# Kernel tuning notes

Hardware: AMD Instinct MI355X
Metric: run time of the kernel (lower is better)

Reference implementation:

```python
import jax, jax.numpy as jnp
import numpy as np

SLOPE = 0.2  # leaky_relu_slope for both LVC block and kernel predictor (passed through)
DILATIONS = (1, 3, 9, 27)
HOP = 256
STRIDE = 8
IN_CH = 32
KSZ = 3  # conv_kernel_size


def conv1d(x, w, b, dilation=1, padding=0):
    # x: (B,C,T), w: (O,I,K) torch layout
    y = jax.lax.conv_general_dilated(
        x, w, window_strides=(1,), padding=[(padding, padding)],
        rhs_dilation=(dilation,), dimension_numbers=('NCH', 'OIH', 'NCH'))
    return y + b[None, :, None]


def conv_transpose1d(x, w, b, stride, padding, output_padding=0):
    # w: torch ConvTranspose1d layout (Cin, Cout, K)
    w_ = jnp.flip(w, -1).transpose(1, 0, 2)  # (Cout, Cin, K)
    K = w.shape[2]
    pad = (K - 1 - padding, K - 1 - padding + output_padding)
    y = jax.lax.conv_general_dilated(
        x, w_, window_strides=(1,), padding=[pad],
        lhs_dilation=(stride,), dimension_numbers=('NCH', 'OIH', 'NCH'))
    return y + b[None, :, None]


def lrelu(x, slope=SLOPE):
    return jnp.where(x >= 0, x, slope * x)


def location_variable_convolution(x, kernel, bias, hop):
    # x: (B,C,T), kernel: (B,C,O,k,L), bias: (B,O,L); T == L*hop; dilation==1 path
    B, C, T = x.shape
    _, _, O, k, L = kernel.shape
    pad = (k - 1) // 2
    xp = jnp.pad(x, ((0, 0), (0, 0), (pad, pad)))
    # gather per-segment sliding windows: (L, hop, k) index into time axis
    idx = (jnp.arange(L)[:, None, None] * hop
           + jnp.arange(hop)[None, :, None]
           + jnp.arange(k)[None, None, :])
    xw = xp[:, :, idx]  # (B, C, L, hop, k)
    o = jnp.einsum('bclsk,bcokl->bols', xw, kernel)  # (B, O, L, hop)
    o = o + bias[:, :, :, None]
    return o.reshape(B, O, L * hop)


def kernel_predictor(spec, kp_in_w, kp_in_b, rb_w1, rb_b1, rb_w2, rb_b2,
                     kern_w, kern_b, bias_w, bias_b):
    B, _, L = spec.shape
    h = conv1d(spec, kp_in_w, kp_in_b, padding=2)  # k=5, pad=2
    for i in range(3):  # num_blocks = 3
        r = h
        h = conv1d(h, rb_w1[i], rb_b1[i], padding=1)
        h = lrelu(h)
        h = conv1d(h, rb_w2[i], rb_b2[i], padding=1)
        h = lrelu(h) + r
    kh = conv1d(h, kern_w, kern_b, padding=1)
    bh = conv1d(h, bias_w, bias_b, padding=1)
    n_layers = len(DILATIONS)
    kernels = kh.reshape(B, n_layers, IN_CH, 2 * IN_CH, KSZ, L)
    biases = bh.reshape(B, n_layers, 2 * IN_CH, L)
    return kernels, biases


def reference(hidden_states, spectrogram, convt_w, convt_b, kp_in_w, kp_in_b,
              rb_w1, rb_b1, rb_w2, rb_b2, kern_w, kern_b, bias_w, bias_b,
              lvc_w, lvc_b):
    h = conv_transpose1d(hidden_states, convt_w, convt_b,
                         stride=STRIDE, padding=STRIDE // 2 + STRIDE % 2,
                         output_padding=STRIDE % 2)
    kernels, biases = kernel_predictor(spectrogram, kp_in_w, kp_in_b,
                                       rb_w1, rb_b1, rb_w2, rb_b2,
                                       kern_w, kern_b, bias_w, bias_b)
    for i, d in enumerate(DILATIONS):
        r = h
        h = lrelu(h)
        h = conv1d(h, lvc_w[i], lvc_b[i], dilation=d, padding=d * (KSZ - 1) // 2)
        h = lrelu(h)
        h = location_variable_convolution(h, kernels[:, i], biases[:, i], HOP)
        h = jax.nn.sigmoid(h[:, :IN_CH, :]) * jnp.tanh(h[:, IN_CH:, :]) + r
    return h


def setup_inputs() -> dict:
    key = jax.random.key(0)
    ks = jax.random.split(key, 12)
    B, COND, L, H = 4, 100, 256, 64
    T = L * HOP  # 65536 output samples
    s = jnp.float32(0.02)
    d = {}
    d['hidden_states'] = jax.random.normal(ks[0], (B, IN_CH, T // STRIDE), jnp.float32)
    d['spectrogram'] = jax.random.normal(ks[1], (B, COND, L), jnp.float32)
    d['convt_w'] = jax.random.normal(ks[2], (IN_CH, IN_CH, 2 * STRIDE), jnp.float32) * s
    d['convt_b'] = jnp.zeros((IN_CH,), jnp.float32)
    d['kp_in_w'] = jax.random.normal(ks[3], (H, COND, 5), jnp.float32) * s
    d['kp_in_b'] = jnp.zeros((H,), jnp.float32)
    d['rb_w1'] = jax.random.normal(ks[4], (3, H, H, 3), jnp.float32) * s
    d['rb_b1'] = jnp.zeros((3, H), jnp.float32)
    d['rb_w2'] = jax.random.normal(ks[5], (3, H, H, 3), jnp.float32) * s
    d['rb_b2'] = jnp.zeros((3, H), jnp.float32)
    KC = IN_CH * 2 * IN_CH * KSZ * len(DILATIONS)  # 24576
    d['kern_w'] = jax.random.normal(ks[6], (KC, H, 3), jnp.float32) * s
    d['kern_b'] = jnp.zeros((KC,), jnp.float32)
    BC = 2 * IN_CH * len(DILATIONS)  # 256
    d['bias_w'] = jax.random.normal(ks[7], (BC, H, 3), jnp.float32) * s
    d['bias_b'] = jnp.zeros((BC,), jnp.float32)
    d['lvc_w'] = jax.random.normal(ks[8], (len(DILATIONS), IN_CH, IN_CH, 3), jnp.float32) * s
    d['lvc_b'] = jnp.zeros((len(DILATIONS), IN_CH), jnp.float32)
    return d
```

## Files before the change

kernel.cpp:

```cpp
#include <hip/hip_runtime.h>
#include <math.h>

#define NB 4
#define T 65536
#define TIN 8192
#define LL 256
#define KCL 6144

__device__ __forceinline__ float lrelu_f(float v) { return v >= 0.f ? v : 0.2f * v; }

union Phase1LDS {
    struct { float xs[32][264]; float wm[64][128]; } cvt;
    struct { float hs[64][56]; float xsp[20][56]; float wt[192][68]; } trk;
};

__global__ void __launch_bounds__(512) phase1(
    const float* __restrict__ x, const float* __restrict__ cw,
    const float* __restrict__ cbias, float* __restrict__ hout,
    const float* __restrict__ spec,
    const float* __restrict__ kp_in_w, const float* __restrict__ kp_in_b,
    const float* __restrict__ rb_w1, const float* __restrict__ rb_b1,
    const float* __restrict__ rb_w2, const float* __restrict__ rb_b2,
    float* __restrict__ kp_h) {
    __shared__ Phase1LDS u;
    const int bid = blockIdx.x;
    const int tid = threadIdx.x;
    const int lane = tid & 63, wv = tid >> 6;

    if (bid < 264) {
        const int bx = bid % 33;
        const int rr = bid / 33;
        const int mtp = rr & 1;
        const int b = rr >> 1;
        const int s0base = bx * 256;
        float (*xs)[264] = u.cvt.xs;
        float (*wm)[128] = u.cvt.wm;

        const float* xb = x + (size_t)b * 32 * TIN;
        for (int idx = tid; idx < 32 * 64; idx += 512) {
            int c = idx >> 6, q = idx & 63;
            int p = s0base + q * 4;
            float4 v = (p + 3 < TIN) ? *(const float4*)(xb + c * TIN + p)
                                     : make_float4(0.f, 0.f, 0.f, 0.f);
            *(float4*)&xs[c][4 + 4 * q] = v;
        }
        if (tid < 32) {
            int p = s0base - 1;
            xs[tid][3] = (p >= 0) ? xb[tid * TIN + p] : 0.f;
        }
        for (int idx = tid; idx < 8192; idx += 512) {
            int i = idx >> 7, mm = idx & 127;
            int oo = mtp * 16 + (mm >> 3), k0 = mm & 7;
            wm[i][mm] = (i < 32) ? cw[i * 512 + oo * 16 + k0]
                                 : cw[(i - 32) * 512 + oo * 16 + k0 + 8];
        }
        __syncthreads();

        float acc[2][8][4];
#pragma unroll
        for (int ol = 0; ol < 2; ++ol) {
            float bo = cbias[mtp * 16 + wv * 2 + ol];
#pragma unroll
            for (int k0 = 0; k0 < 8; ++k0)
#pragma unroll
                for (int si = 0; si < 4; ++si) acc[ol][k0][si] = bo;
        }

        for (int c = 0; c < 32; ++c) {
            float xm1[4], x0[4];
#pragma unroll
            for (int si = 0; si < 4; ++si) {
                xm1[si] = xs[c][lane + si * 64 + 3];
                x0[si]  = xs[c][lane + si * 64 + 4];
            }
            float w0[16], w1[16];
#pragma unroll
            for (int q = 0; q < 4; ++q) {
                *(float4*)&w0[q * 4] = *(const float4*)&wm[c][wv * 16 + q * 4];
                *(float4*)&w1[q * 4] = *(const float4*)&wm[32 + c][wv * 16 + q * 4];
            }
#pragma unroll
            for (int ol = 0; ol < 2; ++ol)
#pragma unroll
                for (int k0 = 0; k0 < 8; ++k0)
#pragma unroll
                    for (int si = 0; si < 4; ++si)
                        acc[ol][k0][si] += x0[si] * w0[ol * 8 + k0] + xm1[si] * w1[ol * 8 + k0];
        }

#pragma unroll
        for (int ol = 0; ol < 2; ++ol) {
            float* ob = hout + ((size_t)b * 32 + mtp * 16 + wv * 2 + ol) * T;
#pragma unroll
            for (int si = 0; si < 4; ++si) {
                int tb = (s0base + lane + si * 64) * 8 - 4;
                if (tb >= 0 && tb < T)
                    *(float4*)(ob + tb) = make_float4(acc[ol][0][si], acc[ol][1][si],
                                                      acc[ol][2][si], acc[ol][3][si]);
                if (tb + 4 >= 0 && tb + 4 < T)
                    *(float4*)(ob + tb + 4) = make_float4(acc[ol][4][si], acc[ol][5][si],
                                                          acc[ol][6][si], acc[ol][7][si]);
            }
        }
        return;
    }

    const int tb = bid - 264;
    const int lq = tb & 7, b = tb >> 3;
    const int j = lane;
    const int oc0 = wv * 8;
    const int l0 = lq * 32;
    const int labs = l0 - 9 + j;
    const bool lvalid = (labs >= 0 && labs < 256);

    float (*hs)[56] = u.trk.hs;
    float (*xsp)[56] = u.trk.xsp;
    float (*wt)[68] = u.trk.wt;

    float pw[24];
    float px[3];

    auto pf_kpin = [&](int cc) {
#pragma unroll
        for (int t = 0; t < 13; ++t) {
            int idx = t * 512 + tid;
            pw[t] = 0.f;
            if (idx < 6400) pw[t] = kp_in_w[(size_t)(idx / 100) * 500 + cc * 100 + (idx % 100)];
        }
    };
    auto wr_kpin = [&]() {
#pragma unroll
        for (int t = 0; t < 13; ++t) {
            int idx = t * 512 + tid;
            if (idx < 6400) wt[idx % 100][idx / 100] = pw[t];
        }
    };
    auto pf_xsp = [&](int cc) {
#pragma unroll
        for (int t = 0; t < 3; ++t) {
            int idx = t * 512 + tid;
            px[t] = 0.f;
            if (idx < 1120) {
                int c = idx / 56, jj = idx - c * 56;
                int l = l0 - 9 + jj;
                if (l >= 0 && l < 256)
                    px[t] = spec[((size_t)b * 100 + cc * 20 + c) * LL + l];
            }
        }
    };
    auto wr_xsp = [&]() {
#pragma unroll
        for (int t = 0; t < 3; ++t) {
            int idx = t * 512 + tid;
            if (idx < 1120) xsp[idx / 56][idx % 56] = px[t];
        }
    };
    auto pf_w192 = [&](const float* src) {
#pragma unroll
        for (int t = 0; t < 24; ++t) pw[t] = src[t * 512 + tid];
    };
    auto wr_w192 = [&]() {
#pragma unroll
        for (int t = 0; t < 24; ++t) {
            int idx = t * 512 + tid;
            wt[idx % 192][idx / 192] = pw[t];
        }
    };
    auto conv64 = [&](int jlo, int jhi, const float* bptr, float* a) {
#pragma unroll
        for (int oi = 0; oi < 8; ++oi) a[oi] = bptr[oc0 + oi];
        if (j >= jlo && j < jhi) {
            for (int c = 0; c < 64; ++c) {
                float x0 = hs[c][j - 1], x1 = hs[c][j], x2 = hs[c][j + 1];
#pragma unroll
                for (int k = 0; k < 3; ++k) {
                    float xk = (k == 0) ? x0 : (k == 1) ? x1 : x2;
                    float w8[8];
                    *(float4*)&w8[0] = *(const float4*)&wt[c * 3 + k][oc0];
                    *(float4*)&w8[4] = *(const float4*)&wt[c * 3 + k][oc0 + 4];
#pragma unroll
                    for (int oi = 0; oi < 8; ++oi) a[oi] += xk * w8[oi];
                }
            }
        }
    };

    pf_kpin(0); pf_xsp(0);
    wr_kpin(); wr_xsp();
    __syncthreads();

    float acc[8];
#pragma unroll
    for (int oi = 0; oi < 8; ++oi) acc[oi] = kp_in_b[oc0 + oi];

    for (int cc = 0; cc < 5; ++cc) {
        if (cc < 4) { pf_kpin(cc + 1); pf_xsp(cc + 1); }
        else        { pf_w192(rb_w1); }
        if (j >= 2 && j < 48) {
            for (int c = 0; c < 20; ++c) {
                float x5[5];
#pragma unroll
                for (int u2 = 0; u2 < 5; ++u2) x5[u2] = xsp[c][j - 2 + u2];
#pragma unroll
                for (int k = 0; k < 5; ++k) {
                    float w8[8];
                    *(float4*)&w8[0] = *(const float4*)&wt[c * 5 + k][oc0];
                    *(float4*)&w8[4] = *(const float4*)&wt[c * 5 + k][oc0 + 4];
#pragma unroll
                    for (int oi = 0; oi < 8; ++oi) acc[oi] += x5[k] * w8[oi];
                }
            }
        }
        if (cc == 4 && j >= 2 && j < 48) {
#pragma unroll
            for (int oi = 0; oi < 8; ++oi) hs[oc0 + oi][j] = lvalid ? acc[oi] : 0.f;
        }
        __syncthreads();
        if (cc < 4) { wr_kpin(); wr_xsp(); }
        else        { wr_w192(); }
        __syncthreads();
    }

    for (int i = 0; i < 3; ++i) {
        const int jlo1 = 3 + 2 * i, jhi1 = 47 - 2 * i;
        const int jlo2 = jlo1 + 1, jhi2 = jhi1 - 1;
        float r[8];
        if (j >= jlo2 && j < jhi2) {
#pragma unroll
            for (int oi = 0; oi < 8; ++oi) r[oi] = hs[oc0 + oi][j];
        }
        pf_w192(rb_w2 + (size_t)i * 12288);
        float a1[8];
        conv64(jlo1, jhi1, rb_b1 + i * 64, a1);
        __syncthreads();
        if (j >= jlo1 && j < jhi1) {
#pragma unroll
            for (int oi = 0; oi < 8; ++oi) hs[oc0 + oi][j] = lvalid ? lrelu_f(a1[oi]) : 0.f;
        }
        wr_w192();
        __syncthreads();
        if (i < 2) pf_w192(rb_w1 + (size_t)(i + 1) * 12288);
        float a2[8];
        conv64(jlo2, jhi2, rb_b2 + i * 64, a2);
        __syncthreads();
        if (j >= jlo2 && j < jhi2) {
#pragma unroll
            for (int oi = 0; oi < 8; ++oi) hs[oc0 + oi][j] = lvalid ? (lrelu_f(a2[oi]) + r[oi]) : 0.f;
        }
        if (i < 2) wr_w192();
        __syncthreads();
    }

    for (int idx = tid; idx < 64 * 32; idx += 512) {
        int c = idx >> 5, jj = idx & 31;
        kp_h[((size_t)b * 64 + c) * LL + l0 + jj] = hs[c][9 + jj];
    }
}

__global__ void __launch_bounds__(256, 3) kern_head(const float* __restrict__ kp_h,
                                                    const float* __restrict__ kw,
                                                    const float* __restrict__ kb,
                                                    const float* __restrict__ bias_w,
                                                    const float* __restrict__ bias_b,
                                                    float* __restrict__ kh,
                                                    float* __restrict__ bh, int layer) {
    const int bx = blockIdx.x, b = blockIdx.y;
    const bool isbias = (bx >= 192);
    const int tid = threadIdx.x, lane = tid & 63, wv = tid >> 6;
    __shared__ float xs[32][264];
    __shared__ float ws[96][36];

    int g = 0, oc0 = 0, ci = 0, kk = 0, ocb0 = 0;
    const float* wsrc;
    size_t wrow0;
    int wstride;
    if (!isbias) {
        g = bx >> 1; oc0 = (bx & 1) * 32;
        ci = g / 3; kk = g - ci * 3;
        wsrc = kw + (size_t)layer * KCL * 192;
        wrow0 = (size_t)((ci * 64 + oc0) * 3 + kk) * 192;
        wstride = 576;
    } else {
        ocb0 = (bx - 192) * 32;
        wsrc = bias_w;
        wrow0 = (size_t)ocb0 * 192;
        wstride = 192;
    }

    float acc[8][4];
#pragma unroll
    for (int oi = 0; oi < 8; ++oi) {
        float bv = isbias ? bias_b[ocb0 + wv * 8 + oi]
                          : kb[layer * KCL + (ci * 64 + oc0 + wv * 8 + oi) * 3 + kk];
#pragma unroll
        for (int si = 0; si < 4; ++si) acc[oi][si] = bv;
    }

    for (int half = 0; half < 2; ++half) {
        const int hc0 = half * 32;
        __syncthreads();
        for (int idx = tid; idx < 32 * 64; idx += 256) {
            int c = idx >> 6, q = idx & 63;
            *(float4*)&xs[c][4 + 4 * q] =
                *(const float4*)(kp_h + ((size_t)b * 64 + hc0 + c) * LL + 4 * q);
        }
        if (tid < 32) { xs[tid][3] = 0.f; xs[tid][260] = 0.f; }
        for (int idx = tid; idx < 3072; idx += 256) {
            int ocl = idx / 96, jj = idx - ocl * 96;
            ws[jj][ocl] = wsrc[wrow0 + (size_t)ocl * wstride + hc0 * 3 + jj];
        }
        __syncthreads();
        for (int c = 0; c < 32; ++c) {
#pragma unroll
            for (int t = 0; t < 3; ++t) {
                float wv8[8];
                *(float4*)&wv8[0] = *(const float4*)&ws[c * 3 + t][wv * 8];
                *(float4*)&wv8[4] = *(const float4*)&ws[c * 3 + t][wv * 8 + 4];
                float xv[4];
#pragma unroll
                for (int si = 0; si < 4; ++si) xv[si] = xs[c][lane + si * 64 + t + 3];
#pragma unroll
                for (int oi = 0; oi < 8; ++oi)
#pragma unroll
                    for (int si = 0; si < 4; ++si)
                        acc[oi][si] += wv8[oi] * xv[si];
            }
        }
    }

    if (!isbias) {
#pragma unroll
        for (int si = 0; si < 4; ++si) {
            int l = lane + si * 64;
            float* op = kh + ((size_t)b * LL + l) * KCL + g * 64 + oc0 + wv * 8;
            *(float4*)(op)     = make_float4(acc[0][si], acc[1][si], acc[2][si], acc[3][si]);
            *(float4*)(op + 4) = make_float4(acc[4][si], acc[5][si], acc[6][si], acc[7][si]);
        }
    } else {
#pragma unroll
        for (int oi = 0; oi < 8; ++oi) {
            float* op = bh + ((size_t)b * 256 + ocb0 + wv * 8 + oi) * LL;
#pragma unroll
            for (int si = 0; si < 4; ++si)
                op[lane + si * 64] = acc[oi][si];
        }
    }
}

__global__ void __launch_bounds__(512, 4) layer_fused(
    const float* __restrict__ kh, const float* __restrict__ bh,
    const float* __restrict__ w, const float* __restrict__ bias,
    const float* __restrict__ hin, float* __restrict__ hout,
    int layer, int dil) {
    const int l = blockIdx.x, b = blockIdx.y;
    const int tid = threadIdx.x, lane = tid & 63, wv = tid >> 6;
    const int t0 = l * 256;
    __shared__ float xh[32][316];
    __shared__ float ks[KCL];
    __shared__ float ws[96][36];

    const float* hb = hin + (size_t)b * 32 * T;
    for (int idx = tid; idx < 32 * 64; idx += 512) {
        int c = idx >> 6, q = idx & 63;
        float4 v = *(const float4*)(hb + (size_t)c * T + t0 + 4 * q);
        *(float4*)&xh[c][32 + 4 * q] = make_float4(lrelu_f(v.x), lrelu_f(v.y),
                                                   lrelu_f(v.z), lrelu_f(v.w));
    }
    for (int idx = tid; idx < 32 * 60; idx += 512) {
        int c = idx / 60, r = idx - c * 60;
        int jj = (r < 32) ? r : (256 + r);
        int t = t0 + jj - 32;
        xh[c][jj] = (t >= 0 && t < T) ? lrelu_f(hb[(size_t)c * T + t]) : 0.f;
    }
    {
        const float4* kp = (const float4*)(kh + ((size_t)b * LL + l) * KCL);
        float4* kd = (float4*)ks;
        for (int idx = tid; idx < KCL / 4; idx += 512) kd[idx] = kp[idx];
    }
    for (int idx = tid; idx < 3072; idx += 512) {
        int oc = idx / 96, ck = idx - oc * 96;
        ws[ck][oc] = w[oc * 96 + ck];
    }
    __syncthreads();

    const int oc4 = wv * 4;
    float yv[5][4];
    {
        float a[5][4];
#pragma unroll
        for (int oi = 0; oi < 4; ++oi) {
            float bv = bias[oc4 + oi];
#pragma unroll
            for (int si = 0; si < 5; ++si) a[si][oi] = bv;
        }
        for (int c = 0; c < 32; ++c) {
#pragma unroll
            for (int k = 0; k < 3; ++k) {
                float4 wq = *(const float4*)&ws[c * 3 + k][oc4];
                float xv[5];
#pragma unroll
                for (int si = 0; si < 5; ++si) {
                    int col = lane + si * 64;
                    int colc = (col < 258) ? col : 257;
                    xv[si] = xh[c][colc + 31 + (k - 1) * dil];
                }
#pragma unroll
                for (int si = 0; si < 5; ++si) {
                    a[si][0] += xv[si] * wq.x;
                    a[si][1] += xv[si] * wq.y;
                    a[si][2] += xv[si] * wq.z;
                    a[si][3] += xv[si] * wq.w;
                }
            }
        }
#pragma unroll
        for (int si = 0; si < 5; ++si) {
            int t = t0 - 1 + lane + si * 64;
            bool tval = (t >= 0 && t < T);
#pragma unroll
            for (int oi = 0; oi < 4; ++oi)
                yv[si][oi] = tval ? lrelu_f(a[si][oi]) : 0.f;
        }
    }
    __syncthreads();

#pragma unroll
    for (int si = 0; si < 5; ++si) {
        int col = lane + si * 64;
        if (col < 258) {
#pragma unroll
            for (int oi = 0; oi < 4; ++oi) xh[oc4 + oi][col + 31] = yv[si][oi];
        }
    }
    __syncthreads();

    const int oc8 = (wv & 3) * 8;
    const int sh  = wv >> 2;
    float acc_a[8][2], acc_g[8][2];
#pragma unroll
    for (int oi = 0; oi < 8; ++oi) {
        float ba = bh[((size_t)b * 256 + layer * 64 + oc8 + oi) * LL + l];
        float bg = bh[((size_t)b * 256 + layer * 64 + 32 + oc8 + oi) * LL + l];
#pragma unroll
        for (int si = 0; si < 2; ++si) { acc_a[oi][si] = ba; acc_g[oi][si] = bg; }
    }

    for (int c = 0; c < 32; ++c) {
#pragma unroll
        for (int k = 0; k < 3; ++k) {
            const float* kr = ks + (c * 3 + k) * 64;
            float wa[8], wg[8];
            *(float4*)&wa[0] = *(const float4*)(kr + oc8);
            *(float4*)&wa[4] = *(const float4*)(kr + oc8 + 4);
            *(float4*)&wg[0] = *(const float4*)(kr + 32 + oc8);
            *(float4*)&wg[4] = *(const float4*)(kr + 32 + oc8 + 4);
            float xv2[2];
#pragma unroll
            for (int si = 0; si < 2; ++si) {
                int s = lane + (sh * 2 + si) * 64;
                xv2[si] = xh[c][s + k + 31];
            }
#pragma unroll
            for (int oi = 0; oi < 8; ++oi)
#pragma unroll
                for (int si = 0; si < 2; ++si) {
                    acc_a[oi][si] += wa[oi] * xv2[si];
                    acc_g[oi][si] += wg[oi] * xv2[si];
                }
        }
    }

#pragma unroll
    for (int oi = 0; oi < 8; ++oi) {
        const float* hip = hin + ((size_t)b * 32 + oc8 + oi) * T + t0;
        float* hop = hout + ((size_t)b * 32 + oc8 + oi) * T + t0;
#pragma unroll
        for (int si = 0; si < 2; ++si) {
            int s = lane + (sh * 2 + si) * 64;
            float a = acc_a[oi][si], g = acc_g[oi][si];
            float sg = 1.f / (1.f + __expf(-a));
            float th = tanhf(g);
            hop[s] = sg * th + hip[s];
        }
    }
}

extern "C" void kernel_launch(void* const* d_in, const int* in_sizes, int n_in,
                              void* d_out, int out_size, void* d_ws, size_t ws_size,
                              hipStream_t stream) {
    const float* hidden  = (const float*)d_in[0];
    const float* spec    = (const float*)d_in[1];
    const float* convt_w = (const float*)d_in[2];
    const float* convt_b = (const float*)d_in[3];
    const float* kp_in_w = (const float*)d_in[4];
    const float* kp_in_b = (const float*)d_in[5];
    const float* rb_w1   = (const float*)d_in[6];
    const float* rb_b1   = (const float*)d_in[7];
    const float* rb_w2   = (const float*)d_in[8];
    const float* rb_b2   = (const float*)d_in[9];
    const float* kern_w  = (const float*)d_in[10];
    const float* kern_b  = (const float*)d_in[11];
    const float* bias_w  = (const float*)d_in[12];
    const float* bias_b  = (const float*)d_in[13];
    const float* lvc_w   = (const float*)d_in[14];
    const float* lvc_b   = (const float*)d_in[15];

    float* wsp = (float*)d_ws;
    float* h_ws     = wsp;
    float* kh_layer = h_ws + (size_t)NB * 32 * T;
    float* bh       = kh_layer + (size_t)NB * LL * KCL;
    float* kp_h     = bh + (size_t)NB * 256 * LL;

    float* h0 = (float*)d_out;
    float* h1 = h_ws;

    phase1<<<dim3(296), 512, 0, stream>>>(hidden, convt_w, convt_b, h0,
                                          spec, kp_in_w, kp_in_b,
                                          rb_w1, rb_b1, rb_w2, rb_b2, kp_h);

    static const int dil[4] = {1, 3, 9, 27};
    float* hin = h0;
    float* hout = h1;
    for (int layer = 0; layer < 4; ++layer) {
        kern_head<<<dim3(layer == 0 ? 200 : 192, NB), 256, 0, stream>>>(
            kp_h, kern_w, kern_b, bias_w, bias_b, kh_layer, bh, layer);
        layer_fused<<<dim3(LL, NB), 512, 0, stream>>>(
            kh_layer, bh, lvc_w + (size_t)layer * 32 * 32 * 3, lvc_b + layer * 32,
            hin, hout, layer, dil[layer]);
        float* tmp = hin; hin = hout; hout = tmp;
    }
}
```

Before: 723.7 us.

## Remap kernel-predictor threads to output channels and split LVC pre-conv by channel halves

The kernel-predictor tail of phase1 now assigns one output channel per lane and eight time positions per wave. Weights are read straight from global memory into registers in place of the LDS-staged transposed weight buffer, and the software prefetch pipeline is removed. The LVC-layer pre-convolution is restructured so that each wave computes 8 output channels over half the input channels, and the two halves are reduced through LDS. The aim is fewer LDS weight reads and better register reuse, at the cost of heavy register pressure (96-float weight arrays) and extra barriers.

```diff
diff --git a/kernel.cpp b/kernel.cpp
--- a/kernel.cpp
+++ b/kernel.cpp
@@ -9,9 +9,9 @@
 
 __device__ __forceinline__ float lrelu_f(float v) { return v >= 0.f ? v : 0.2f * v; }
 
-union Phase1LDS {
+union __align__(16) Phase1LDS {
     struct { float xs[32][264]; float wm[64][128]; } cvt;
-    struct { float hs[64][56]; float xsp[20][56]; float wt[192][68]; } trk;
+    struct { float hs[64][68]; float xsp[20][68]; } trk;
 };
 
 __global__ void __launch_bounds__(512) phase1(
@@ -105,155 +105,161 @@
         return;
     }
 
-    const int tb = bid - 264;
-    const int lq = tb & 7, b = tb >> 3;
-    const int j = lane;
-    const int oc0 = wv * 8;
+    const int tb2 = bid - 264;
+    const int lq = tb2 & 7, b = tb2 >> 3;
+    const int oc = lane;
+    const int j0 = wv * 8;
     const int l0 = lq * 32;
-    const int labs = l0 - 9 + j;
-    const bool lvalid = (labs >= 0 && labs < 256);
-
-    float (*hs)[56] = u.trk.hs;
-    float (*xsp)[56] = u.trk.xsp;
-    float (*wt)[68] = u.trk.wt;
-
-    float pw[24];
-    float px[3];
-
-    auto pf_kpin = [&](int cc) {
-#pragma unroll
-        for (int t = 0; t < 13; ++t) {
-            int idx = t * 512 + tid;
-            pw[t] = 0.f;
-            if (idx < 6400) pw[t] = kp_in_w[(size_t)(idx / 100) * 500 + cc * 100 + (idx % 100)];
-        }
-    };
-    auto wr_kpin = [&]() {
-#pragma unroll
-        for (int t = 0; t < 13; ++t) {
-            int idx = t * 512 + tid;
-            if (idx < 6400) wt[idx % 100][idx / 100] = pw[t];
-        }
-    };
-    auto pf_xsp = [&](int cc) {
-#pragma unroll
-        for (int t = 0; t < 3; ++t) {
-            int idx = t * 512 + tid;
-            px[t] = 0.f;
-            if (idx < 1120) {
-                int c = idx / 56, jj = idx - c * 56;
-                int l = l0 - 9 + jj;
-                if (l >= 0 && l < 256)
-                    px[t] = spec[((size_t)b * 100 + cc * 20 + c) * LL + l];
-            }
-        }
-    };
-    auto wr_xsp = [&]() {
-#pragma unroll
-        for (int t = 0; t < 3; ++t) {
-            int idx = t * 512 + tid;
-            if (idx < 1120) xsp[idx / 56][idx % 56] = px[t];
-        }
-    };
-    auto pf_w192 = [&](const float* src) {
-#pragma unroll
-        for (int t = 0; t < 24; ++t) pw[t] = src[t * 512 + tid];
-    };
-    auto wr_w192 = [&]() {
-#pragma unroll
-        for (int t = 0; t < 24; ++t) {
-            int idx = t * 512 + tid;
-            wt[idx % 192][idx / 192] = pw[t];
-        }
-    };
-    auto conv64 = [&](int jlo, int jhi, const float* bptr, float* a) {
-#pragma unroll
-        for (int oi = 0; oi < 8; ++oi) a[oi] = bptr[oc0 + oi];
-        if (j >= jlo && j < jhi) {
-            for (int c = 0; c < 64; ++c) {
-                float x0 = hs[c][j - 1], x1 = hs[c][j], x2 = hs[c][j + 1];
-#pragma unroll
-                for (int k = 0; k < 3; ++k) {
-                    float xk = (k == 0) ? x0 : (k == 1) ? x1 : x2;
-                    float w8[8];
-                    *(float4*)&w8[0] = *(const float4*)&wt[c * 3 + k][oc0];
-                    *(float4*)&w8[4] = *(const float4*)&wt[c * 3 + k][oc0 + 4];
-#pragma unroll
-                    for (int oi = 0; oi < 8; ++oi) a[oi] += xk * w8[oi];
-                }
-            }
-        }
-    };
-
-    pf_kpin(0); pf_xsp(0);
-    wr_kpin(); wr_xsp();
+    const bool active = (j0 < 48);
+
+    float (*hs)[68] = u.trk.hs;
+    float (*xsp)[68] = u.trk.xsp;
+
+    for (int idx = tid; idx < 64 * 68; idx += 512) ((float*)hs)[idx] = 0.f;
+
+    float acc[8];
+#pragma unroll
+    for (int q = 0; q < 8; ++q) acc[q] = kp_in_b[oc];
+
+    for (int cc = 0; cc < 5; ++cc) {
+        __syncthreads();
+        for (int idx = tid; idx < 20 * 68; idx += 512) {
+            int c = idx / 68, v = idx - c * 68;
+            int jj = v - 4;
+            int l = l0 - 9 + jj;
+            float val = 0.f;
+            if (jj >= 0 && jj < 56 && l >= 0 && l < 256)
+                val = spec[((size_t)b * 100 + cc * 20 + c) * LL + l];
+            xsp[c][v] = val;
+        }
+        __syncthreads();
+        if (active) {
+#pragma unroll
+            for (int half = 0; half < 2; ++half) {
+                const int c0 = half ? 12 : 0;
+                const int nc = half ? 8 : 12;
+                float wreg[60];
+                const float* wp = kp_in_w + (size_t)oc * 500 + cc * 100 + c0 * 5;
+#pragma unroll
+                for (int q4 = 0; q4 < 15; ++q4)
+                    if (q4 * 4 < nc * 5)
+                        *(float4*)&wreg[q4 * 4] = *(const float4*)(wp + q4 * 4);
+#pragma unroll
+                for (int c = 0; c < nc; ++c) {
+                    float xw[16];
+                    *(float4*)&xw[0]  = *(const float4*)&xsp[c0 + c][j0];
+                    *(float4*)&xw[4]  = *(const float4*)&xsp[c0 + c][j0 + 4];
+                    *(float4*)&xw[8]  = *(const float4*)&xsp[c0 + c][j0 + 8];
+                    *(float4*)&xw[12] = *(const float4*)&xsp[c0 + c][j0 + 12];
+#pragma unroll
+                    for (int q = 0; q < 8; ++q)
+#pragma unroll
+                        for (int k = 0; k < 5; ++k)
+                            acc[q] += wreg[c * 5 + k] * xw[q + k + 2];
+                }
+            }
+        }
+        __syncthreads();
+    }
+    if (active) {
+#pragma unroll
+        for (int q = 0; q < 8; ++q) {
+            int j = j0 + q;
+            if (j >= 2 && j < 48) {
+                int labs = l0 - 9 + j;
+                hs[oc][2 + j] = (labs >= 0 && labs < 256) ? acc[q] : 0.f;
+            }
+        }
+    }
     __syncthreads();
-
-    float acc[8];
-#pragma unroll
-    for (int oi = 0; oi < 8; ++oi) acc[oi] = kp_in_b[oc0 + oi];
-
-    for (int cc = 0; cc < 5; ++cc) {
-        if (cc < 4) { pf_kpin(cc + 1); pf_xsp(cc + 1); }
-        else        { pf_w192(rb_w1); }
-        if (j >= 2 && j < 48) {
-            for (int c = 0; c < 20; ++c) {
-                float x5[5];
-#pragma unroll
-                for (int u2 = 0; u2 < 5; ++u2) x5[u2] = xsp[c][j - 2 + u2];
-#pragma unroll
-                for (int k = 0; k < 5; ++k) {
-                    float w8[8];
-                    *(float4*)&w8[0] = *(const float4*)&wt[c * 5 + k][oc0];
-                    *(float4*)&w8[4] = *(const float4*)&wt[c * 5 + k][oc0 + 4];
-#pragma unroll
-                    for (int oi = 0; oi < 8; ++oi) acc[oi] += x5[k] * w8[oi];
-                }
-            }
-        }
-        if (cc == 4 && j >= 2 && j < 48) {
-#pragma unroll
-            for (int oi = 0; oi < 8; ++oi) hs[oc0 + oi][j] = lvalid ? acc[oi] : 0.f;
-        }
-        __syncthreads();
-        if (cc < 4) { wr_kpin(); wr_xsp(); }
-        else        { wr_w192(); }
-        __syncthreads();
-    }
 
     for (int i = 0; i < 3; ++i) {
         const int jlo1 = 3 + 2 * i, jhi1 = 47 - 2 * i;
         const int jlo2 = jlo1 + 1, jhi2 = jhi1 - 1;
-        float r[8];
-        if (j >= jlo2 && j < jhi2) {
-#pragma unroll
-            for (int oi = 0; oi < 8; ++oi) r[oi] = hs[oc0 + oi][j];
-        }
-        pf_w192(rb_w2 + (size_t)i * 12288);
-        float a1[8];
-        conv64(jlo1, jhi1, rb_b1 + i * 64, a1);
-        __syncthreads();
-        if (j >= jlo1 && j < jhi1) {
-#pragma unroll
-            for (int oi = 0; oi < 8; ++oi) hs[oc0 + oi][j] = lvalid ? lrelu_f(a1[oi]) : 0.f;
-        }
-        wr_w192();
-        __syncthreads();
-        if (i < 2) pf_w192(rb_w1 + (size_t)(i + 1) * 12288);
+        float r[8], a1[8];
+        if (active) {
+#pragma unroll
+            for (int q = 0; q < 8; ++q) {
+                a1[q] = rb_b1[i * 64 + oc];
+                r[q]  = hs[oc][2 + j0 + q];
+            }
+#pragma unroll
+            for (int half = 0; half < 2; ++half) {
+                float wreg[96];
+                const float* wp = rb_w1 + (size_t)i * 12288 + (size_t)oc * 192 + half * 96;
+#pragma unroll
+                for (int q4 = 0; q4 < 24; ++q4)
+                    *(float4*)&wreg[q4 * 4] = *(const float4*)(wp + q4 * 4);
+#pragma unroll
+                for (int c = 0; c < 32; ++c) {
+                    const int cg = half * 32 + c;
+                    float xw[12];
+                    *(float4*)&xw[0] = *(const float4*)&hs[cg][j0];
+                    *(float4*)&xw[4] = *(const float4*)&hs[cg][j0 + 4];
+                    *(float4*)&xw[8] = *(const float4*)&hs[cg][j0 + 8];
+#pragma unroll
+                    for (int q = 0; q < 8; ++q)
+#pragma unroll
+                        for (int k = 0; k < 3; ++k)
+                            a1[q] += wreg[c * 3 + k] * xw[q + k + 1];
+                }
+            }
+        }
+        __syncthreads();
+        if (active) {
+#pragma unroll
+            for (int q = 0; q < 8; ++q) {
+                int j = j0 + q;
+                if (j >= jlo1 && j < jhi1) {
+                    int labs = l0 - 9 + j;
+                    hs[oc][2 + j] = (labs >= 0 && labs < 256) ? lrelu_f(a1[q]) : 0.f;
+                }
+            }
+        }
+        __syncthreads();
         float a2[8];
-        conv64(jlo2, jhi2, rb_b2 + i * 64, a2);
-        __syncthreads();
-        if (j >= jlo2 && j < jhi2) {
-#pragma unroll
-            for (int oi = 0; oi < 8; ++oi) hs[oc0 + oi][j] = lvalid ? (lrelu_f(a2[oi]) + r[oi]) : 0.f;
-        }
-        if (i < 2) wr_w192();
-        __syncthreads();
-    }
-
-    for (int idx = tid; idx < 64 * 32; idx += 512) {
+        if (active) {
+#pragma unroll
+            for (int q = 0; q < 8; ++q) a2[q] = rb_b2[i * 64 + oc];
+#pragma unroll
+            for (int half = 0; half < 2; ++half) {
+                float wreg[96];
+                const float* wp = rb_w2 + (size_t)i * 12288 + (size_t)oc * 192 + half * 96;
+#pragma unroll
+                for (int q4 = 0; q4 < 24; ++q4)
+                    *(float4*)&wreg[q4 * 4] = *(const float4*)(wp + q4 * 4);
+#pragma unroll
+                for (int c = 0; c < 32; ++c) {
+                    const int cg = half * 32 + c;
+                    float xw[12];
+                    *(float4*)&xw[0] = *(const float4*)&hs[cg][j0];
+                    *(float4*)&xw[4] = *(const float4*)&hs[cg][j0 + 4];
+                    *(float4*)&xw[8] = *(const float4*)&hs[cg][j0 + 8];
+#pragma unroll
+                    for (int q = 0; q < 8; ++q)
+#pragma unroll
+                        for (int k = 0; k < 3; ++k)
+                            a2[q] += wreg[c * 3 + k] * xw[q + k + 1];
+                }
+            }
+        }
+        __syncthreads();
+        if (active) {
+#pragma unroll
+            for (int q = 0; q < 8; ++q) {
+                int j = j0 + q;
+                if (j >= jlo2 && j < jhi2) {
+                    int labs = l0 - 9 + j;
+                    hs[oc][2 + j] = (labs >= 0 && labs < 256) ? (lrelu_f(a2[q]) + r[q]) : 0.f;
+                }
+            }
+        }
+        __syncthreads();
+    }
+
+    for (int idx = tid; idx < 2048; idx += 512) {
         int c = idx >> 5, jj = idx & 31;
-        kp_h[((size_t)b * 64 + c) * LL + l0 + jj] = hs[c][9 + jj];
+        kp_h[((size_t)b * 64 + c) * LL + l0 + jj] = hs[c][11 + jj];
     }
 }
 
@@ -383,53 +389,61 @@
     }
     __syncthreads();
 
-    const int oc4 = wv * 4;
-    float yv[5][4];
-    {
-        float a[5][4];
-#pragma unroll
-        for (int oi = 0; oi < 4; ++oi) {
-            float bv = bias[oc4 + oi];
-#pragma unroll
-            for (int si = 0; si < 5; ++si) a[si][oi] = bv;
-        }
-        for (int c = 0; c < 32; ++c) {
-#pragma unroll
-            for (int k = 0; k < 3; ++k) {
-                float4 wq = *(const float4*)&ws[c * 3 + k][oc4];
-                float xv[5];
-#pragma unroll
-                for (int si = 0; si < 5; ++si) {
-                    int col = lane + si * 64;
-                    int colc = (col < 258) ? col : 257;
-                    xv[si] = xh[c][colc + 31 + (k - 1) * dil];
-                }
-#pragma unroll
-                for (int si = 0; si < 5; ++si) {
-                    a[si][0] += xv[si] * wq.x;
-                    a[si][1] += xv[si] * wq.y;
-                    a[si][2] += xv[si] * wq.z;
-                    a[si][3] += xv[si] * wq.w;
-                }
-            }
-        }
+    const int oc8b = (wv & 3) * 8;
+    const int chb  = wv >> 2;
+    float p[8][5];
+#pragma unroll
+    for (int oi = 0; oi < 8; ++oi)
+#pragma unroll
+        for (int si = 0; si < 5; ++si) p[oi][si] = 0.f;
+
+    for (int c = chb * 16; c < chb * 16 + 16; ++c) {
+#pragma unroll
+        for (int k = 0; k < 3; ++k) {
+            float w8[8];
+            *(float4*)&w8[0] = *(const float4*)&ws[c * 3 + k][oc8b];
+            *(float4*)&w8[4] = *(const float4*)&ws[c * 3 + k][oc8b + 4];
+            float xv[5];
+#pragma unroll
+            for (int si = 0; si < 5; ++si) {
+                int col = lane + si * 64;
+                int colc = (col < 258) ? col : 257;
+                xv[si] = xh[c][colc + 31 + (k - 1) * dil];
+            }
+#pragma unroll
+            for (int oi = 0; oi < 8; ++oi)
+#pragma unroll
+                for (int si = 0; si < 5; ++si)
+                    p[oi][si] += w8[oi] * xv[si];
+        }
+    }
+    __syncthreads();
+
+    if (chb == 0) {
 #pragma unroll
         for (int si = 0; si < 5; ++si) {
-            int t = t0 - 1 + lane + si * 64;
-            bool tval = (t >= 0 && t < T);
-#pragma unroll
-            for (int oi = 0; oi < 4; ++oi)
-                yv[si][oi] = tval ? lrelu_f(a[si][oi]) : 0.f;
+            int col = lane + si * 64;
+            if (col < 258) {
+#pragma unroll
+                for (int oi = 0; oi < 8; ++oi)
+                    xh[oc8b + oi][col + 31] = p[oi][si] + bias[oc8b + oi];
+            }
         }
     }
     __syncthreads();
-
-#pragma unroll
-    for (int si = 0; si < 5; ++si) {
-        int col = lane + si * 64;
-        if (col < 258) {
-#pragma unroll
-            for (int oi = 0; oi < 4; ++oi) xh[oc4 + oi][col + 31] = yv[si][oi];
+    if (chb == 1) {
+#pragma unroll
+        for (int si = 0; si < 5; ++si) {
+            int col = lane + si * 64;
+            if (col < 258) {
+                int t = t0 - 1 + col;
+                bool tv = (t >= 0 && t < T);
+#pragma unroll
+                for (int oi = 0; oi < 8; ++oi) {
+                    float v = xh[oc8b + oi][col + 31] + p[oi][si];
+                    xh[oc8b + oi][col + 31] = tv ? lrelu_f(v) : 0.f;
+                }
+            }
         }
     }
     __syncthreads();
```

Measured after the change: 762.6 us. 5.4% more time.

## Enlarge per-thread register tiles in kern_head and layer_fused, split dilated conv by channel halves

Applied to the files above, without the earlier changes.

kern_head now runs 128 threads per block, each computing 16 output channels instead of 8, and preloads the three shifted input taps per channel into registers. In layer_fused the dilated conv is split across two channel halves that are reduced through shared memory, giving each wave 8 output channels. The location-variable conv is then done by only 4 waves, each covering 4 time samples, so weights loaded from LDS are reused more. The goal is fewer LDS loads per FMA, at the cost of more registers, extra barriers, and half the waves sitting idle during the final stage.

```diff
diff --git a/kernel.cpp b/kernel.cpp
--- a/kernel.cpp
+++ b/kernel.cpp
@@ -105,8 +105,8 @@
         return;
     }
 
-    const int tb = bid - 264;
-    const int lq = tb & 7, b = tb >> 3;
+    const int tb2 = bid - 264;
+    const int lq = tb2 & 7, b = tb2 >> 3;
     const int j = lane;
     const int oc0 = wv * 8;
     const int l0 = lq * 32;
@@ -257,16 +257,17 @@
     }
 }
 
-__global__ void __launch_bounds__(256, 3) kern_head(const float* __restrict__ kp_h,
-                                                    const float* __restrict__ kw,
-                                                    const float* __restrict__ kb,
-                                                    const float* __restrict__ bias_w,
-                                                    const float* __restrict__ bias_b,
-                                                    float* __restrict__ kh,
-                                                    float* __restrict__ bh, int layer) {
+__global__ void __launch_bounds__(128) kern_head(const float* __restrict__ kp_h,
+                                                 const float* __restrict__ kw,
+                                                 const float* __restrict__ kb,
+                                                 const float* __restrict__ bias_w,
+                                                 const float* __restrict__ bias_b,
+                                                 float* __restrict__ kh,
+                                                 float* __restrict__ bh, int layer) {
     const int bx = blockIdx.x, b = blockIdx.y;
     const bool isbias = (bx >= 192);
-    const int tid = threadIdx.x, lane = tid & 63, wv = tid >> 6;
+    const int tid = threadIdx.x, lane = tid & 63, wvk = tid >> 6;
+    const int ocl0 = wvk * 16;
     __shared__ float xs[32][264];
     __shared__ float ws[96][36];
 
@@ -287,11 +288,11 @@
         wstride = 192;
     }
 
-    float acc[8][4];
-#pragma unroll
-    for (int oi = 0; oi < 8; ++oi) {
-        float bv = isbias ? bias_b[ocb0 + wv * 8 + oi]
-                          : kb[layer * KCL + (ci * 64 + oc0 + wv * 8 + oi) * 3 + kk];
+    float acc[16][4];
+#pragma unroll
+    for (int oi = 0; oi < 16; ++oi) {
+        float bv = isbias ? bias_b[ocb0 + ocl0 + oi]
+                          : kb[layer * KCL + (ci * 64 + oc0 + ocl0 + oi) * 3 + kk];
 #pragma unroll
         for (int si = 0; si < 4; ++si) acc[oi][si] = bv;
     }
@@ -299,31 +300,35 @@
     for (int half = 0; half < 2; ++half) {
         const int hc0 = half * 32;
         __syncthreads();
-        for (int idx = tid; idx < 32 * 64; idx += 256) {
+        for (int idx = tid; idx < 32 * 64; idx += 128) {
             int c = idx >> 6, q = idx & 63;
             *(float4*)&xs[c][4 + 4 * q] =
                 *(const float4*)(kp_h + ((size_t)b * 64 + hc0 + c) * LL + 4 * q);
         }
         if (tid < 32) { xs[tid][3] = 0.f; xs[tid][260] = 0.f; }
-        for (int idx = tid; idx < 3072; idx += 256) {
+        for (int idx = tid; idx < 3072; idx += 128) {
             int ocl = idx / 96, jj = idx - ocl * 96;
             ws[jj][ocl] = wsrc[wrow0 + (size_t)ocl * wstride + hc0 * 3 + jj];
         }
         __syncthreads();
         for (int c = 0; c < 32; ++c) {
+            float xr[4][3];
+#pragma unroll
+            for (int si = 0; si < 4; ++si)
+#pragma unroll
+                for (int t = 0; t < 3; ++t)
+                    xr[si][t] = xs[c][lane + si * 64 + t + 3];
 #pragma unroll
             for (int t = 0; t < 3; ++t) {
-                float wv8[8];
-                *(float4*)&wv8[0] = *(const float4*)&ws[c * 3 + t][wv * 8];
-                *(float4*)&wv8[4] = *(const float4*)&ws[c * 3 + t][wv * 8 + 4];
-                float xv[4];
-#pragma unroll
-                for (int si = 0; si < 4; ++si) xv[si] = xs[c][lane + si * 64 + t + 3];
-#pragma unroll
-                for (int oi = 0; oi < 8; ++oi)
+                float w16[16];
+#pragma unroll
+                for (int q = 0; q < 4; ++q)
+                    *(float4*)&w16[q * 4] = *(const float4*)&ws[c * 3 + t][ocl0 + q * 4];
+#pragma unroll
+                for (int oi = 0; oi < 16; ++oi)
 #pragma unroll
                     for (int si = 0; si < 4; ++si)
-                        acc[oi][si] += wv8[oi] * xv[si];
+                        acc[oi][si] += w16[oi] * xr[si][t];
             }
         }
     }
@@ -332,14 +337,16 @@
 #pragma unroll
         for (int si = 0; si < 4; ++si) {
             int l = lane + si * 64;
-            float* op = kh + ((size_t)b * LL + l) * KCL + g * 64 + oc0 + wv * 8;
-            *(float4*)(op)     = make_float4(acc[0][si], acc[1][si], acc[2][si], acc[3][si]);
-            *(float4*)(op + 4) = make_float4(acc[4][si], acc[5][si], acc[6][si], acc[7][si]);
+            float* op = kh + ((size_t)b * LL + l) * KCL + g * 64 + oc0 + ocl0;
+#pragma unroll
+            for (int q = 0; q < 4; ++q)
+                *(float4*)(op + q * 4) = make_float4(acc[q * 4][si], acc[q * 4 + 1][si],
+                                                     acc[q * 4 + 2][si], acc[q * 4 + 3][si]);
         }
     } else {
 #pragma unroll
-        for (int oi = 0; oi < 8; ++oi) {
-            float* op = bh + ((size_t)b * 256 + ocb0 + wv * 8 + oi) * LL;
+        for (int oi = 0; oi < 16; ++oi) {
+            float* op = bh + ((size_t)b * 256 + ocb0 + ocl0 + oi) * LL;
 #pragma unroll
             for (int si = 0; si < 4; ++si)
                 op[lane + si * 64] = acc[oi][si];
@@ -383,104 +390,113 @@
     }
     __syncthreads();
 
-    const int oc4 = wv * 4;
-    float yv[5][4];
-    {
-        float a[5][4];
-#pragma unroll
-        for (int oi = 0; oi < 4; ++oi) {
-            float bv = bias[oc4 + oi];
-#pragma unroll
-            for (int si = 0; si < 5; ++si) a[si][oi] = bv;
-        }
+    const int oc8b = (wv & 3) * 8;
+    const int chb  = wv >> 2;
+    float p[8][5];
+#pragma unroll
+    for (int oi = 0; oi < 8; ++oi)
+#pragma unroll
+        for (int si = 0; si < 5; ++si) p[oi][si] = 0.f;
+
+    for (int c = chb * 16; c < chb * 16 + 16; ++c) {
+#pragma unroll
+        for (int k = 0; k < 3; ++k) {
+            float w8[8];
+            *(float4*)&w8[0] = *(const float4*)&ws[c * 3 + k][oc8b];
+            *(float4*)&w8[4] = *(const float4*)&ws[c * 3 + k][oc8b + 4];
+            float xv[5];
+#pragma unroll
+            for (int si = 0; si < 5; ++si) {
+                int col = lane + si * 64;
+                int colc = (col < 258) ? col : 257;
+                xv[si] = xh[c][colc + 31 + (k - 1) * dil];
+            }
+#pragma unroll
+            for (int oi = 0; oi < 8; ++oi)
+#pragma unroll
+                for (int si = 0; si < 5; ++si)
+                    p[oi][si] += w8[oi] * xv[si];
+        }
+    }
+    __syncthreads();
+
+    if (chb == 0) {
+#pragma unroll
+        for (int si = 0; si < 5; ++si) {
+            int col = lane + si * 64;
+            if (col < 258) {
+#pragma unroll
+                for (int oi = 0; oi < 8; ++oi)
+                    xh[oc8b + oi][col + 31] = p[oi][si] + bias[oc8b + oi];
+            }
+        }
+    }
+    __syncthreads();
+    if (chb == 1) {
+#pragma unroll
+        for (int si = 0; si < 5; ++si) {
+            int col = lane + si * 64;
+            if (col < 258) {
+                int t = t0 - 1 + col;
+                bool tv = (t >= 0 && t < T);
+#pragma unroll
+                for (int oi = 0; oi < 8; ++oi) {
+                    float v = xh[oc8b + oi][col + 31] + p[oi][si];
+                    xh[oc8b + oi][col + 31] = tv ? lrelu_f(v) : 0.f;
+                }
+            }
+        }
+    }
+    __syncthreads();
+
+    if (wv < 4) {
+        const int oc8 = wv * 8;
+        float acc_a[8][4], acc_g[8][4];
+#pragma unroll
+        for (int oi = 0; oi < 8; ++oi) {
+            float ba = bh[((size_t)b * 256 + layer * 64 + oc8 + oi) * LL + l];
+            float bg = bh[((size_t)b * 256 + layer * 64 + 32 + oc8 + oi) * LL + l];
+#pragma unroll
+            for (int si = 0; si < 4; ++si) { acc_a[oi][si] = ba; acc_g[oi][si] = bg; }
+        }
+
         for (int c = 0; c < 32; ++c) {
+            float xr[4][3];
+#pragma unroll
+            for (int si = 0; si < 4; ++si)
+#pragma unroll
+                for (int k = 0; k < 3; ++k)
+                    xr[si][k] = xh[c][lane + si * 64 + k + 31];
 #pragma unroll
             for (int k = 0; k < 3; ++k) {
-                float4 wq = *(const float4*)&ws[c * 3 + k][oc4];
-                float xv[5];
-#pragma unroll
-                for (int si = 0; si < 5; ++si) {
-                    int col = lane + si * 64;
-                    int colc = (col < 258) ? col : 257;
-                    xv[si] = xh[c][colc + 31 + (k - 1) * dil];
-                }
-#pragma unroll
-                for (int si = 0; si < 5; ++si) {
-                    a[si][0] += xv[si] * wq.x;
-                    a[si][1] += xv[si] * wq.y;
-                    a[si][2] += xv[si] * wq.z;
-                    a[si][3] += xv[si] * wq.w;
-                }
-            }
-        }
-#pragma unroll
-        for (int si = 0; si < 5; ++si) {
-            int t = t0 - 1 + lane + si * 64;
-            bool tval = (t >= 0 && t < T);
-#pragma unroll
-            for (int oi = 0; oi < 4; ++oi)
-                yv[si][oi] = tval ? lrelu_f(a[si][oi]) : 0.f;
-        }
-    }
-    __syncthreads();
-
-#pragma unroll
-    for (int si = 0; si < 5; ++si) {
-        int col = lane + si * 64;
-        if (col < 258) {
-#pragma unroll
-            for (int oi = 0; oi < 4; ++oi) xh[oc4 + oi][col + 31] = yv[si][oi];
-        }
-    }
-    __syncthreads();
-
-    const int oc8 = (wv & 3) * 8;
-    const int sh  = wv >> 2;
-    float acc_a[8][2], acc_g[8][2];
-#pragma unroll
-    for (int oi = 0; oi < 8; ++oi) {
-        float ba = bh[((size_t)b * 256 + layer * 64 + oc8 + oi) * LL + l];
-        float bg = bh[((size_t)b * 256 + layer * 64 + 32 + oc8 + oi) * LL + l];
-#pragma unroll
-        for (int si = 0; si < 2; ++si) { acc_a[oi][si] = ba; acc_g[oi][si] = bg; }
-    }
-
-    for (int c = 0; c < 32; ++c) {
-#pragma unroll
-        for (int k = 0; k < 3; ++k) {
-            const float* kr = ks + (c * 3 + k) * 64;
-            float wa[8], wg[8];
-            *(float4*)&wa[0] = *(const float4*)(kr + oc8);
-            *(float4*)&wa[4] = *(const float4*)(kr + oc8 + 4);
-            *(float4*)&wg[0] = *(const float4*)(kr + 32 + oc8);
-            *(float4*)&wg[4] = *(const float4*)(kr + 32 + oc8 + 4);
-            float xv2[2];
-#pragma unroll
-            for (int si = 0; si < 2; ++si) {
-                int s = lane + (sh * 2 + si) * 64;
-                xv2[si] = xh[c][s + k + 31];
-            }
-#pragma unroll
-            for (int oi = 0; oi < 8; ++oi)
-#pragma unroll
-                for (int si = 0; si < 2; ++si) {
-                    acc_a[oi][si] += wa[oi] * xv2[si];
-                    acc_g[oi][si] += wg[oi] * xv2[si];
-                }
-        }
-    }
-
-#pragma unroll
-    for (int oi = 0; oi < 8; ++oi) {
-        const float* hip = hin + ((size_t)b * 32 + oc8 + oi) * T + t0;
-        float* hop = hout + ((size_t)b * 32 + oc8 + oi) * T + t0;
-#pragma unroll
-        for (int si = 0; si < 2; ++si) {
-            int s = lane + (sh * 2 + si) * 64;
-            float a = acc_a[oi][si], g = acc_g[oi][si];
-            float sg = 1.f / (1.f + __expf(-a));
-            float th = tanhf(g);
-            hop[s] = sg * th + hip[s];
+                const float* kr = ks + (c * 3 + k) * 64;
+                float wa[8], wg[8];
+                *(float4*)&wa[0] = *(const float4*)(kr + oc8);
+                *(float4*)&wa[4] = *(const float4*)(kr + oc8 + 4);
+                *(float4*)&wg[0] = *(const float4*)(kr + 32 + oc8);
+                *(float4*)&wg[4] = *(const float4*)(kr + 32 + oc8 + 4);
+#pragma unroll
+                for (int oi = 0; oi < 8; ++oi)
+#pragma unroll
+                    for (int si = 0; si < 4; ++si) {
+                        acc_a[oi][si] += wa[oi] * xr[si][k];
+                        acc_g[oi][si] += wg[oi] * xr[si][k];
+                    }
+            }
+        }
+
+#pragma unroll
+        for (int oi = 0; oi < 8; ++oi) {
+            const float* hip = hin + ((size_t)b * 32 + oc8 + oi) * T + t0;
+            float* hop = hout + ((size_t)b * 32 + oc8 + oi) * T + t0;
+#pragma unroll
+            for (int si = 0; si < 4; ++si) {
+                int s = lane + si * 64;
+                float a = acc_a[oi][si], g = acc_g[oi][si];
+                float sg = 1.f / (1.f + __expf(-a));
+                float th = tanhf(g);
+                hop[s] = sg * th + hip[s];
+            }
         }
     }
 }
@@ -522,7 +538,7 @@
     float* hin = h0;
     float* hout = h1;
     for (int layer = 0; layer < 4; ++layer) {
-        kern_head<<<dim3(layer == 0 ? 200 : 192, NB), 256, 0, stream>>>(
+        kern_head<<<dim3(layer == 0 ? 200 : 192, NB), 128, 0, stream>>>(
             kp_h, kern_w, kern_b, bias_w, bias_b, kh_layer, bh, layer);
         layer_fused<<<dim3(LL, NB), 512, 0, stream>>>(
             kh_layer, bh, lvc_w + (size_t)layer * 32 * 32 * 3, lvc_b + layer * 32,
```

Result: slower. 788.5 us (+9.0%).
